# Kernel tuning notes

Measured on AMD Instinct MI355X. Metric: run time of the kernel, lower is better.

Reference implementation:

```python
import jax, jax.numpy as jnp
import numpy as np

LN_EPS = 1e-5

def layer_norm(x, w, b):
    mu = jnp.mean(x, axis=-1, keepdims=True)
    var = jnp.mean(jnp.square(x - mu), axis=-1, keepdims=True)
    return (x - mu) * jax.lax.rsqrt(var + LN_EPS) * w + b

def setup_inputs() -> dict:
    key = jax.random.key(0)
    ks = jax.random.split(key, 8)
    B, F, Q, D = 8, 4096, 64, 1024
    H, DH = 16, 64
    inner = H * DH
    s = 1.0 / np.sqrt(D)
    return {
        "features": jax.random.normal(ks[0], (B, F, D), jnp.float32),
        "latents": jax.random.normal(ks[1], (B, Q, D), jnp.float32),
        "key_attention_mask": jax.random.randint(ks[2], (B, F), 0, 2, jnp.int32),
        "ln_m_w": jnp.ones((D,), jnp.float32),
        "ln_m_b": jnp.zeros((D,), jnp.float32),
        "ln_l_w": jnp.ones((D,), jnp.float32),
        "ln_l_b": jnp.zeros((D,), jnp.float32),
        "Wq": jax.random.normal(ks[3], (D, inner), jnp.float32) * s,
        "Wk": jax.random.normal(ks[4], (D, inner), jnp.float32) * s,
        "Wv": jax.random.normal(ks[5], (D, inner), jnp.float32) * s,
        "Wo": jax.random.normal(ks[6], (inner, D), jnp.float32) * (1.0 / np.sqrt(inner)),
    }

def reference(features, latents, key_attention_mask, ln_m_w, ln_m_b, ln_l_w, ln_l_b, Wq, Wk, Wv, Wo):
    H, DH = 16, 64
    B, F, D = features.shape
    Q = latents.shape[1]
    scale = DH ** (-0.5)

    x = layer_norm(features, ln_m_w, ln_m_b)          # [B,F,D]
    lat = layer_norm(latents, ln_l_w, ln_l_b)          # [B,Q,D]

    q = (lat @ Wq).reshape(B, Q, H, DH).transpose(0, 2, 1, 3)   # [B,H,Q,DH]
    kv_in = jnp.concatenate([x, lat], axis=1)                    # [B,F+Q,D]
    k = (kv_in @ Wk).reshape(B, F + Q, H, DH).transpose(0, 2, 1, 3)
    v = (kv_in @ Wv).reshape(B, F + Q, H, DH).transpose(0, 2, 1, 3)

    q = q * scale
    sim = jnp.einsum('bhqd,bhfd->bhqf', q, k)                    # [B,H,Q,F+Q]

    full_mask = jnp.concatenate(
        [key_attention_mask, jnp.ones((B, Q), key_attention_mask.dtype)], axis=1)  # [B,F+Q]
    sim = jnp.where(full_mask[:, None, None, :] == 0, -jnp.inf, sim)

    sim = sim - jax.lax.stop_gradient(jnp.max(sim, axis=-1, keepdims=True))
    alphas = jax.nn.softmax(sim, axis=-1)
    out = jnp.einsum('bhqf,bhfv->bhqv', alphas, v)               # [B,H,Q,DH]
    out = out.transpose(0, 2, 1, 3).reshape(B, Q, H * DH)        # [B,Q,inner]
    return out @ Wo                                              # [B,Q,D]
```

## Files before the change

### kernel.cpp

```cpp
#include <hip/hip_runtime.h>
#include <hip/hip_bf16.h>

#define B_    8
#define F_    4096
#define Qn    64
#define Dm    1024
#define Hh    16
#define DHn   64
#define FQ    4160
#define ROWS_KV 33280
#define ROWS_F  32768
#define KS    13
#define CHPB  5
#define KVOFF ((size_t)ROWS_KV * 1024)

typedef __bf16 v8bf __attribute__((ext_vector_type(8)));
typedef __bf16 v4bf __attribute__((ext_vector_type(4)));
typedef float  v4f  __attribute__((ext_vector_type(4)));

__device__ inline void gl_lds16(const __bf16* g, __bf16* l) {
  __builtin_amdgcn_global_load_lds((__attribute__((address_space(1))) void*)(g),
                                   (__attribute__((address_space(3))) void*)(l),
                                   16, 0, 0);
}

__device__ inline bool is_bf16_inputs(const void* mw) {
  return ((const unsigned int*)mw)[0] != 0x3F800000u;
}

__global__ __launch_bounds__(256) void prep_kernel(
    const void* __restrict__ feat, const void* __restrict__ lat,
    const void* __restrict__ mw, const void* __restrict__ mb,
    const void* __restrict__ lw, const void* __restrict__ lb,
    __bf16* __restrict__ kv_bf, __bf16* __restrict__ lat_bf,
    const void* __restrict__ w0, const void* __restrict__ w1,
    const void* __restrict__ w2, const void* __restrict__ w3,
    __bf16* __restrict__ t0, __bf16* __restrict__ t1,
    __bf16* __restrict__ t2, __bf16* __restrict__ t3)
{
  bool bf = is_bf16_inputs(mw);
  __shared__ __bf16 tile[32][33];
  int bid = blockIdx.x;
  int tid = threadIdx.x;

  if (bid >= 8320) {
    int tb = bid - 8320;
    int z = tb >> 10, rem = tb & 1023;
    int bxx = rem & 31, byy = rem >> 5;
    int tx = tid & 31, ty = tid >> 5;
    const void* src; __bf16* dst;
    switch (z) {
      case 0: src = w0; dst = t0; break;
      case 1: src = w1; dst = t1; break;
      case 2: src = w2; dst = t2; break;
      default: src = w3; dst = t3; break;
    }
    int x = bxx * 32 + tx;
    #pragma unroll
    for (int j = 0; j < 4; ++j) {
      int y = byy * 32 + ty + j * 8;
      size_t e = (size_t)y * 1024 + x;
      float v = bf ? (float)((const __bf16*)src)[e] : ((const float*)src)[e];
      tile[ty + j * 8][tx] = (__bf16)v;
    }
    __syncthreads();
    int x2 = byy * 32 + tx;
    #pragma unroll
    for (int j = 0; j < 4; ++j) {
      int y2 = bxx * 32 + ty + j * 8;
      dst[(size_t)y2 * 1024 + x2] = tile[tx][ty + j * 8];
    }
    return;
  }

  int wave = tid >> 6, lane = tid & 63;
  int r = bid * 4 + wave;
  const void *rowp, *w, *g;
  __bf16 *dst, *dst2 = nullptr;
  size_t rowoff;
  if (r < ROWS_F) {
    rowoff = (size_t)r * Dm; rowp = feat; w = mw; g = mb;
    int b = r >> 12, f = r & (F_ - 1);
    dst = kv_bf + ((size_t)b * FQ + f) * Dm;
  } else {
    int r2 = r - ROWS_F;
    rowoff = (size_t)r2 * Dm; rowp = lat; w = lw; g = lb;
    int b = r2 >> 6, q = r2 & 63;
    dst  = kv_bf + ((size_t)b * FQ + F_ + q) * Dm;
    dst2 = lat_bf + (size_t)r2 * Dm;
  }
  float xs[16], ws_[16], gs[16];
  if (bf) {
    const __bf16* rp = (const __bf16*)rowp + rowoff;
    const __bf16* wp = (const __bf16*)w;
    const __bf16* gp = (const __bf16*)g;
    #pragma unroll
    for (int g2 = 0; g2 < 2; ++g2) {
      int base = g2 * 512 + lane * 8;
      v8bf X = *(const v8bf*)(rp + base);
      v8bf W = *(const v8bf*)(wp + base);
      v8bf G = *(const v8bf*)(gp + base);
      #pragma unroll
      for (int j = 0; j < 8; ++j) {
        xs[g2*8+j] = (float)X[j]; ws_[g2*8+j] = (float)W[j]; gs[g2*8+j] = (float)G[j];
      }
    }
  } else {
    const float* rp = (const float*)rowp + rowoff;
    const float* wp = (const float*)w;
    const float* gp = (const float*)g;
    #pragma unroll
    for (int g4 = 0; g4 < 4; ++g4) {
      int base = g4 * 256 + lane * 4;
      float4 X = *(const float4*)(rp + base);
      float4 W = *(const float4*)(wp + base);
      float4 G = *(const float4*)(gp + base);
      xs[g4*4]=X.x; xs[g4*4+1]=X.y; xs[g4*4+2]=X.z; xs[g4*4+3]=X.w;
      ws_[g4*4]=W.x; ws_[g4*4+1]=W.y; ws_[g4*4+2]=W.z; ws_[g4*4+3]=W.w;
      gs[g4*4]=G.x; gs[g4*4+1]=G.y; gs[g4*4+2]=G.z; gs[g4*4+3]=G.w;
    }
  }
  float s = 0.f, ss = 0.f;
  #pragma unroll
  for (int j = 0; j < 16; ++j) { s += xs[j]; ss += xs[j] * xs[j]; }
  #pragma unroll
  for (int off = 32; off > 0; off >>= 1) {
    s  += __shfl_xor(s, off, 64);
    ss += __shfl_xor(ss, off, 64);
  }
  float mean = s * (1.f / 1024.f);
  float var  = ss * (1.f / 1024.f) - mean * mean;
  float rs = rsqrtf(var + 1e-5f);
  float os[16];
  #pragma unroll
  for (int j = 0; j < 16; ++j) os[j] = (xs[j] - mean) * rs * ws_[j] + gs[j];
  if (bf) {
    #pragma unroll
    for (int g2 = 0; g2 < 2; ++g2) {
      int base = g2 * 512 + lane * 8;
      v8bf O;
      #pragma unroll
      for (int j = 0; j < 8; ++j) O[j] = (__bf16)os[g2*8+j];
      *(v8bf*)(dst + base) = O;
      if (dst2) *(v8bf*)(dst2 + base) = O;
    }
  } else {
    #pragma unroll
    for (int g4 = 0; g4 < 4; ++g4) {
      int base = g4 * 256 + lane * 4;
      v4bf O;
      #pragma unroll
      for (int j = 0; j < 4; ++j) O[j] = (__bf16)os[g4*4+j];
      *(v4bf*)(dst + base) = O;
      if (dst2) *(v4bf*)(dst2 + base) = O;
    }
  }
}


#define BAR() asm volatile("s_barrier" ::: "memory")

#define PH(Q) do { \
  BAR(); \
  asm volatile("s_waitcnt lgkmcnt(0)" ::: "memory"); \
  __builtin_amdgcn_s_setprio(1); \
  Q; \
  __builtin_amdgcn_s_setprio(0); \
  BAR(); \
} while (0)

#define PHV(Q) do { \
  BAR(); \
  asm volatile("s_waitcnt lgkmcnt(0)" ::: "memory"); \
  __builtin_amdgcn_s_setprio(1); \
  Q; \
  __builtin_amdgcn_s_setprio(0); \
  asm volatile("s_waitcnt vmcnt(4)" ::: "memory"); \
  BAR(); \
} while (0)

#define QUAD(MB, NB, BF) do { \
  _Pragma("unroll") \
  for (int m_ = 0; m_ < 4; ++m_) { \
    _Pragma("unroll") \
    for (int n_ = 0; n_ < 2; ++n_) { \
      _Pragma("unroll") \
      for (int k_ = 0; k_ < 2; ++k_) { \
        acc[(MB) + m_][(NB) + n_] = __builtin_amdgcn_mfma_f32_16x16x32_bf16( \
            af[m_][k_], BF[n_][k_], acc[(MB) + m_][(NB) + n_], 0, 0, 0); \
      } } } } while (0)

#define LDA8(BB, ROFF) do { \
  _Pragma("unroll") \
  for (int m_ = 0; m_ < 4; ++m_) { \
    _Pragma("unroll") \
    for (int k_ = 0; k_ < 2; ++k_) { \
      const int r_ = (ROFF) + m_ * 16 + lm; \
      af[m_][k_] = *(const v8bf*)(aB[BB] + ((r_ << 7) + ((k_ * 64 + kcb) ^ ((r_ & 7) << 4)))); \
    } } } while (0)

#define LDB4(BB, DST, NOFF) do { \
  _Pragma("unroll") \
  for (int n_ = 0; n_ < 2; ++n_) { \
    _Pragma("unroll") \
    for (int k_ = 0; k_ < 2; ++k_) { \
      const int r_ = bq + (NOFF) + n_ * 16 + lm; \
      DST[n_][k_] = *(const v8bf*)(bB[BB] + ((r_ << 7) + ((k_ * 64 + kcb) ^ ((r_ & 7) << 4)))); \
    } } } while (0)

#define STAGE_A(BB, H, K0) do { \
  gl_lds16(asrc + (size_t)(H) * 131072 + (K0),         (__bf16*)(ldsw + ((BB) * 4 + (H)) * 16384)); \
  gl_lds16(asrc + (size_t)(H) * 131072 + (K0) + 65536, (__bf16*)(ldsw + ((BB) * 4 + (H)) * 16384 + 8192)); \
} while (0)

#define STAGE_B(BB, H, K0) do { \
  gl_lds16(bsrc + (size_t)(H) * 131072 + (K0),         (__bf16*)(ldsw + ((BB) * 4 + 2 + (H)) * 16384)); \
  gl_lds16(bsrc + (size_t)(H) * 131072 + (K0) + 65536, (__bf16*)(ldsw + ((BB) * 4 + 2 + (H)) * 16384 + 8192)); \
} while (0)

__global__ __launch_bounds__(512, 2) void gemm_kv8_kernel(
    const __bf16* __restrict__ A, const __bf16* __restrict__ lat,
    const __bf16* __restrict__ BtKV,
    __bf16* __restrict__ KVb, __bf16* __restrict__ Qmb)
{
  __shared__ __align__(16) char ldsm[131072];
  const int tid = threadIdx.x;
  const int lane = tid & 63, wave = tid >> 6;
  const int wm = wave >> 2, wn = wave & 3;
  const int lm = lane & 15, l4 = lane >> 4;
  const int kcb = l4 << 4;
  const int bq = (wn & 1) << 6;

  const int r0 = (wave << 3) + (lane >> 3);
  const int xc = ((lane & 7) ^ (lane >> 3)) << 3;
  char* const ldsw = ldsm + tid * 16;

  if (blockIdx.x >= 1024) {
    int qid = blockIdx.x - 1024;
    int m0q, n0q;
    const __bf16* aq;
    if (qid < 64) {
      int tt = 1024 + (qid & 15);
      m0q = ((tt >> 3) << 8) + (qid >> 4) * 64;
      n0q = (tt & 7) << 8;
      aq = A;
    } else {
      int qq = qid - 64;
      m0q = (((qq >> 2) & 1) << 8) + (qq >> 3) * 64;
      n0q = 2048 + ((qq & 3) << 8);
      aq = lat;
    }
    const __bf16* qasrc = aq + (size_t)(m0q + r0) * 1024 + xc;
    const __bf16* bsrc  = BtKV + (size_t)(n0q + r0) * 1024 + xc;
    const char* const bB[1] = { ldsm + (2 + (wn >> 1)) * 16384 };

    v4f qac[2][4];
    #pragma unroll
    for (int i = 0; i < 2; ++i)
      #pragma unroll
      for (int j = 0; j < 4; ++j) qac[i][j] = (v4f){0.f, 0.f, 0.f, 0.f};

    for (int k0 = 0; k0 < 1024; k0 += 64) {
      __syncthreads();
      gl_lds16(qasrc + k0, (__bf16*)ldsw);
      STAGE_B(0, 0, k0);
      STAGE_B(0, 1, k0);
      __syncthreads();
      v8bf a2[2][2], qlo[2][2], qhi[2][2];
      #pragma unroll
      for (int m_ = 0; m_ < 2; ++m_)
        #pragma unroll
        for (int k_ = 0; k_ < 2; ++k_) {
          const int r_ = wm * 32 + m_ * 16 + lm;
          a2[m_][k_] = *(const v8bf*)(ldsm + ((r_ << 7) + ((k_ * 64 + kcb) ^ ((r_ & 7) << 4))));
        }
      LDB4(0, qlo, 0);
      LDB4(0, qhi, 32);
      #pragma unroll
      for (int m_ = 0; m_ < 2; ++m_)
        #pragma unroll
        for (int n_ = 0; n_ < 2; ++n_)
          #pragma unroll
          for (int k_ = 0; k_ < 2; ++k_) {
            qac[m_][n_]     = __builtin_amdgcn_mfma_f32_16x16x32_bf16(a2[m_][k_], qlo[n_][k_], qac[m_][n_], 0, 0, 0);
            qac[m_][n_ + 2] = __builtin_amdgcn_mfma_f32_16x16x32_bf16(a2[m_][k_], qhi[n_][k_], qac[m_][n_ + 2], 0, 0, 0);
          }
    }

    if (n0q >= 2048) {
      #pragma unroll
      for (int m_ = 0; m_ < 2; ++m_)
        #pragma unroll
        for (int n = 0; n < 4; ++n) {
          int col = n0q + (wn << 6) + n * 16 + lm;
          int h = (col >> 6) & 15, dh = col & 63;
          #pragma unroll
          for (int reg = 0; reg < 4; ++reg) {
            int row = m0q + wm * 32 + m_ * 16 + l4 * 4 + reg;
            int b = row >> 6, q = row & 63;
            Qmb[((size_t)(b * Hh + h) * 64 + q) * 64 + dh] = (__bf16)qac[m_][n][reg];
          }
        }
    } else if (n0q >= 1024) {
      #pragma unroll
      for (int m_ = 0; m_ < 2; ++m_)
        #pragma unroll
        for (int n = 0; n < 4; ++n) {
          int col = n0q + (wn << 6) + n * 16 + lm;
          int h = (col >> 6) & 15, dh = col & 63;
          int f0 = m0q + wm * 32 + m_ * 16 + l4 * 4;
          int b = f0 / FQ, f = f0 - b * FQ;
          v4bf pv;
          #pragma unroll
          for (int reg = 0; reg < 4; ++reg) pv[reg] = (__bf16)qac[m_][n][reg];
          *(v4bf*)(KVb + KVOFF + ((size_t)(b * Hh + h) * 64 + dh) * FQ + f) = pv;
        }
    } else {
      #pragma unroll
      for (int m_ = 0; m_ < 2; ++m_)
        #pragma unroll
        for (int n = 0; n < 4; ++n) {
          int col = n0q + (wn << 6) + n * 16 + lm;
          int h = (col >> 6) & 15, dh = col & 63;
          #pragma unroll
          for (int reg = 0; reg < 4; ++reg) {
            int row = m0q + wm * 32 + m_ * 16 + l4 * 4 + reg;
            int b = row / FQ, f = row - b * FQ;
            KVb[((size_t)(b * Hh + h) * FQ + f) * 64 + dh] = (__bf16)qac[m_][n][reg];
          }
        }
    }
    return;
  }

  const int wg = (blockIdx.x & 7) * 128 + (blockIdx.x >> 3);
  const int n0 = (wg & 7) << 8;
  const int m0 = (wg >> 3) << 8;

  const __bf16* asrc = A    + (size_t)(m0 + r0) * 1024 + xc;
  const __bf16* bsrc = BtKV + (size_t)(n0 + r0) * 1024 + xc;
  const char* const aB[2] = { ldsm + wm * 16384, ldsm + (4 + wm) * 16384 };
  const char* const bB[2] = { ldsm + (2 + (wn >> 1)) * 16384,
                              ldsm + (6 + (wn >> 1)) * 16384 };

  v4f acc[8][4];
  #pragma unroll
  for (int i = 0; i < 8; ++i)
    #pragma unroll
    for (int j = 0; j < 4; ++j) acc[i][j] = (v4f){0.f, 0.f, 0.f, 0.f};
  v8bf af[4][2], blo[2][2], bhi[2][2];

  STAGE_A(0, 0, 0); STAGE_A(0, 1, 0);
  STAGE_B(0, 0, 0); STAGE_B(0, 1, 0);
  STAGE_B(1, 0, 64); STAGE_B(1, 1, 64);
  asm volatile("s_waitcnt vmcnt(4)" ::: "memory");
  BAR();

  #pragma unroll 1
  for (int it = 0; it < 8; ++it) {
    const int kA1 = (2 * it + 1) << 6;
    const int kT0 = (it < 7) ? ((2 * it + 2) << 6) : 0;
    const int kT1 = (it < 7) ? ((2 * it + 3) << 6) : 0;

    LDA8(0, 0); LDB4(0, blo, 0);
    STAGE_A(1, 0, kA1);
    PH(QUAD(0, 0, blo));

    LDB4(0, bhi, 32);
    STAGE_A(1, 1, kA1);
    PH(QUAD(0, 2, bhi));

    LDA8(0, 64);
    STAGE_B(0, 0, kT0);
    PH(QUAD(4, 2, bhi));

    STAGE_B(0, 1, kT0);
    PHV(QUAD(4, 0, blo));

    LDA8(1, 0); LDB4(1, blo, 0);
    STAGE_A(0, 0, kT0);
    PH(QUAD(0, 0, blo));

    LDB4(1, bhi, 32);
    STAGE_A(0, 1, kT0);
    PH(QUAD(0, 2, bhi));

    LDA8(1, 64);
    STAGE_B(1, 0, kT1);
    PH(QUAD(4, 2, bhi));

    STAGE_B(1, 1, kT1);
    PHV(QUAD(4, 0, blo));
  }

  const int rb_l = wm << 7;
  const int cb_l = wn << 6;

  if (n0 >= 1024) {
    __syncthreads();
    #pragma unroll
    for (int m = 0; m < 8; ++m)
      #pragma unroll
      for (int n = 0; n < 4; ++n)
        #pragma unroll
        for (int reg = 0; reg < 4; ++reg) {
          int rl = rb_l + m * 16 + l4 * 4 + reg;
          int cl = cb_l + n * 16 + lm;
          int byt = (cl << 9) + ((rl << 1) ^ (((cl >> 2) & 7) << 5));
          *(__bf16*)(ldsm + byt) = (__bf16)acc[m][n][reg];
        }
    __syncthreads();
    {
      const int g = tid >> 4, s = tid & 15;
      #pragma unroll
      for (int p = 0; p < 16; ++p) {
        int d = p * 32 + g;
        int cl = d >> 1, hf = d & 1;
        int byt = (cl << 9) + ((((hf << 8) + (s << 4))) ^ (((cl >> 2) & 7) << 5));
        v8bf val = *(const v8bf*)(ldsm + byt);
        int col = n0 + cl;
        int h = (col >> 6) & 15, dh = col & 63;
        int row = m0 + (hf << 7) + (s << 3);
        int b = row / FQ, f = row - b * FQ;
        *(v8bf*)(KVb + KVOFF + ((size_t)(b * Hh + h) * 64 + dh) * FQ + f) = val;
      }
    }
  } else {
    __syncthreads();
    #pragma unroll
    for (int m = 0; m < 8; ++m)
      #pragma unroll
      for (int n = 0; n < 4; ++n)
        #pragma unroll
        for (int reg = 0; reg < 4; ++reg) {
          int rl = rb_l + m * 16 + l4 * 4 + reg;
          int cl = cb_l + n * 16 + lm;
          int byt = (rl << 9) + ((cl << 1) ^ (((rl >> 2) & 7) << 5));
          *(__bf16*)(ldsm + byt) = (__bf16)acc[m][n][reg];
        }
    __syncthreads();
    {
      const int g = tid >> 3, s = tid & 7;
      #pragma unroll
      for (int p = 0; p < 16; ++p) {
        int d = p * 64 + g;
        int hl = d >> 8, fl = d & 255;
        int byt = (fl << 9) + ((((hl << 7) + (s << 4))) ^ (((fl >> 2) & 7) << 5));
        v8bf val = *(const v8bf*)(ldsm + byt);
        int row = m0 + fl;
        int b = row / FQ, f = row - b * FQ;
        int h = ((n0 + (hl << 6)) >> 6) & 15;
        *(v8bf*)(KVb + ((size_t)(b * Hh + h) * FQ + f) * 64 + (s << 3)) = val;
      }
    }
  }
}

__global__ __launch_bounds__(256) void gemm2_kernel(
    const __bf16* __restrict__ A, const __bf16* __restrict__ Bt,
    void* __restrict__ C, int mode, int out_follow,
    const void* __restrict__ mw)
{
  int obf = out_follow ? (is_bf16_inputs(mw) ? 1 : 0) : 1;

  __shared__ __align__(16) __bf16 As0[128 * 32];
  __shared__ __align__(16) __bf16 As1[128 * 32];
  __shared__ __align__(16) __bf16 Bs0[128 * 32];
  __shared__ __align__(16) __bf16 Bs1[128 * 32];
  int tid = threadIdx.x;
  int lane = tid & 63, wave = tid >> 6;
  int wm = wave >> 1, wn = wave & 1;
  int m0 = blockIdx.y * 128, n0 = blockIdx.x * 128;
  int lm = lane & 15, lk = (lane >> 4) << 3;

  v4f acc[4][4];
  #pragma unroll
  for (int i = 0; i < 4; ++i)
    #pragma unroll
    for (int j = 0; j < 4; ++j) acc[i][j] = (v4f){0.f, 0.f, 0.f, 0.f};

  int c0 = tid, c1 = tid + 256;
  const __bf16* a0p = A  + (size_t)(m0 + (c0 >> 2)) * 1024 + ((c0 & 3) << 3);
  const __bf16* a1p = A  + (size_t)(m0 + (c1 >> 2)) * 1024 + ((c1 & 3) << 3);
  const __bf16* b0p = Bt + (size_t)(n0 + (c0 >> 2)) * 1024 + ((c0 & 3) << 3);
  const __bf16* b1p = Bt + (size_t)(n0 + (c1 >> 2)) * 1024 + ((c1 & 3) << 3);

  for (int k0 = 0; k0 < 1024; k0 += 64) {
    __syncthreads();
    gl_lds16(a0p + k0,      &As0[c0 * 8]);
    gl_lds16(a1p + k0,      &As0[c1 * 8]);
    gl_lds16(a0p + k0 + 32, &As1[c0 * 8]);
    gl_lds16(a1p + k0 + 32, &As1[c1 * 8]);
    gl_lds16(b0p + k0,      &Bs0[c0 * 8]);
    gl_lds16(b1p + k0,      &Bs0[c1 * 8]);
    gl_lds16(b0p + k0 + 32, &Bs1[c0 * 8]);
    gl_lds16(b1p + k0 + 32, &Bs1[c1 * 8]);
    __syncthreads();
    {
      v8bf a[4], b[4];
      #pragma unroll
      for (int i = 0; i < 4; ++i) a[i] = *(const v8bf*)&As0[(wm * 64 + i * 16 + lm) * 32 + lk];
      #pragma unroll
      for (int j = 0; j < 4; ++j) b[j] = *(const v8bf*)&Bs0[(wn * 64 + j * 16 + lm) * 32 + lk];
      #pragma unroll
      for (int i = 0; i < 4; ++i)
        #pragma unroll
        for (int j = 0; j < 4; ++j)
          acc[i][j] = __builtin_amdgcn_mfma_f32_16x16x32_bf16(a[i], b[j], acc[i][j], 0, 0, 0);
    }
    {
      v8bf a[4], b[4];
      #pragma unroll
      for (int i = 0; i < 4; ++i) a[i] = *(const v8bf*)&As1[(wm * 64 + i * 16 + lm) * 32 + lk];
      #pragma unroll
      for (int j = 0; j < 4; ++j) b[j] = *(const v8bf*)&Bs1[(wn * 64 + j * 16 + lm) * 32 + lk];
      #pragma unroll
      for (int i = 0; i < 4; ++i)
        #pragma unroll
        for (int j = 0; j < 4; ++j)
          acc[i][j] = __builtin_amdgcn_mfma_f32_16x16x32_bf16(a[i], b[j], acc[i][j], 0, 0, 0);
    }
  }

  #pragma unroll
  for (int i = 0; i < 4; ++i)
    #pragma unroll
    for (int j = 0; j < 4; ++j) {
      int col = n0 + wn * 64 + j * 16 + lm;
      #pragma unroll
      for (int reg = 0; reg < 4; ++reg) {
        int row = m0 + wm * 64 + i * 16 + (lane >> 4) * 4 + reg;
        size_t idx;
        if (mode == 0) {
          idx = (size_t)row * 1024 + col;
        } else {
          int bb = row >> 6; int qq = row & 63;
          idx = ((size_t)(bb * Hh + (col >> 6)) * 64 + qq) * 64 + (col & 63);
        }
        float v = acc[i][j][reg];
        if (obf) ((__bf16*)C)[idx] = (__bf16)v;
        else     ((float*)C)[idx]  = v;
      }
    }
}

__global__ __launch_bounds__(256) void attn_part_kernel(
    const __bf16* __restrict__ Qm, const __bf16* __restrict__ K,
    const __bf16* __restrict__ Vt, const int* __restrict__ mask,
    float* __restrict__ Opart, float2* __restrict__ ml)
{
  __shared__ __align__(16) __bf16 qs[64 * 72];
  __shared__ __align__(16) __bf16 ks[64 * 72];
  __shared__ __align__(16) __bf16 vts[64 * 72];
  __shared__ __align__(16) __bf16 ps[64 * 72];
  __shared__ float msb[64];

  int tid = threadIdx.x;
  int lane = tid & 63, wave = tid >> 6;
  int ksb = blockIdx.x;
  int bh = blockIdx.y;
  int b = bh >> 4;
  int lm = lane & 15, lq = lane >> 4;

  const __bf16* qsrc = Qm + (size_t)bh * 64 * 64;
  #pragma unroll
  for (int i = 0; i < 2; ++i) {
    int e = (tid + 256 * i) * 8;
    int row = e >> 6, c = e & 63;
    *(v8bf*)&qs[row * 72 + c] = *(const v8bf*)(qsrc + e);
  }

  float mrow[4], lrow[4];
  v4f acco[4];
  #pragma unroll
  for (int r = 0; r < 4; ++r) { mrow[r] = -1e30f; lrow[r] = 0.f; }
  #pragma unroll
  for (int s = 0; s < 4; ++s) acco[s] = (v4f){0.f, 0.f, 0.f, 0.f};

  const __bf16* kbase = K + (size_t)bh * FQ * 64;
  const __bf16* vbase = Vt + (size_t)bh * 64 * FQ;
  const int* maskb = mask + b * F_;

  for (int cc = 0; cc < CHPB; ++cc) {
    int chunk = ksb * CHPB + cc;
    __syncthreads();
    const __bf16* kc = kbase + (size_t)chunk * 4096;
    const __bf16* vc = vbase + chunk * 64;
    #pragma unroll
    for (int i = 0; i < 2; ++i) {
      int e = (tid + 256 * i) * 8;
      int row = e >> 6, c = e & 63;
      *(v8bf*)&ks[row * 72 + c]  = *(const v8bf*)(kc + e);
      *(v8bf*)&vts[row * 72 + c] = *(const v8bf*)(vc + (size_t)row * FQ + c);
    }
    if (tid < 64) {
      int kidx = chunk * 64 + tid;
      msb[tid] = (kidx < F_) ? (maskb[kidx] != 0 ? 0.f : -1e30f) : 0.f;
    }
    __syncthreads();

    v8bf aq0 = *(const v8bf*)&qs[(wave * 16 + lm) * 72 + lq * 8];
    v8bf aq1 = *(const v8bf*)&qs[(wave * 16 + lm) * 72 + lq * 8 + 32];
    v4f sf[4];
    #pragma unroll
    for (int s = 0; s < 4; ++s) {
      v8bf bk0 = *(const v8bf*)&ks[(s * 16 + lm) * 72 + lq * 8];
      v8bf bk1 = *(const v8bf*)&ks[(s * 16 + lm) * 72 + lq * 8 + 32];
      v4f z = (v4f){0.f, 0.f, 0.f, 0.f};
      z = __builtin_amdgcn_mfma_f32_16x16x32_bf16(aq0, bk0, z, 0, 0, 0);
      z = __builtin_amdgcn_mfma_f32_16x16x32_bf16(aq1, bk1, z, 0, 0, 0);
      sf[s] = z;
    }
    float bias[4];
    #pragma unroll
    for (int s = 0; s < 4; ++s) bias[s] = msb[s * 16 + lm];
    #pragma unroll
    for (int s = 0; s < 4; ++s)
      #pragma unroll
      for (int r = 0; r < 4; ++r)
        sf[s][r] = sf[s][r] * 0.125f + bias[s];

    #pragma unroll
    for (int r = 0; r < 4; ++r) {
      float mx = fmaxf(fmaxf(sf[0][r], sf[1][r]), fmaxf(sf[2][r], sf[3][r]));
      #pragma unroll
      for (int off = 1; off < 16; off <<= 1) mx = fmaxf(mx, __shfl_xor(mx, off, 64));
      float mN = fmaxf(mrow[r], mx);
      float alpha = __expf(mrow[r] - mN);
      mrow[r] = mN;
      float ls = 0.f;
      #pragma unroll
      for (int s = 0; s < 4; ++s) { float p = __expf(sf[s][r] - mN); sf[s][r] = p; ls += p; }
      #pragma unroll
      for (int off = 1; off < 16; off <<= 1) ls += __shfl_xor(ls, off, 64);
      lrow[r] = lrow[r] * alpha + ls;
      #pragma unroll
      for (int s = 0; s < 4; ++s) acco[s][r] *= alpha;
    }

    #pragma unroll
    for (int s = 0; s < 4; ++s)
      #pragma unroll
      for (int r = 0; r < 4; ++r)
        ps[(wave * 16 + lq * 4 + r) * 72 + s * 16 + lm] = (__bf16)sf[s][r];

    v8bf ap0 = *(const v8bf*)&ps[(wave * 16 + lm) * 72 + lq * 8];
    v8bf ap1 = *(const v8bf*)&ps[(wave * 16 + lm) * 72 + lq * 8 + 32];
    #pragma unroll
    for (int s = 0; s < 4; ++s) {
      v8bf bv0 = *(const v8bf*)&vts[(s * 16 + lm) * 72 + lq * 8];
      v8bf bv1 = *(const v8bf*)&vts[(s * 16 + lm) * 72 + lq * 8 + 32];
      acco[s] = __builtin_amdgcn_mfma_f32_16x16x32_bf16(ap0, bv0, acco[s], 0, 0, 0);
      acco[s] = __builtin_amdgcn_mfma_f32_16x16x32_bf16(ap1, bv1, acco[s], 0, 0, 0);
    }
  }

  float* Ob = Opart + (((size_t)ksb * 128 + bh) * 64) * 64;
  #pragma unroll
  for (int s = 0; s < 4; ++s)
    #pragma unroll
    for (int r = 0; r < 4; ++r) {
      int q = wave * 16 + lq * 4 + r;
      Ob[q * 64 + s * 16 + lm] = acco[s][r];
    }
  if (lm == 0) {
    #pragma unroll
    for (int r = 0; r < 4; ++r) {
      int q = wave * 16 + lq * 4 + r;
      ml[((size_t)ksb * 128 + bh) * 64 + q] = make_float2(mrow[r], lrow[r]);
    }
  }
}

__global__ __launch_bounds__(256) void attn_comb_kernel(
    const float* __restrict__ Opart, const float2* __restrict__ ml,
    __bf16* __restrict__ attnb)
{
  int bh = blockIdx.x;
  int b = bh >> 4, h = bh & 15;
  int t = threadIdx.x;
  int q = t >> 2, cg = (t & 3) * 16;

  float m_[KS], l_[KS];
  float M = -1e30f;
  #pragma unroll
  for (int k = 0; k < KS; ++k) {
    float2 p = ml[((size_t)k * 128 + bh) * 64 + q];
    m_[k] = p.x; l_[k] = p.y;
    M = fmaxf(M, p.x);
  }
  float L = 0.f;
  #pragma unroll
  for (int k = 0; k < KS; ++k) L += l_[k] * __expf(m_[k] - M);
  float o[16];
  #pragma unroll
  for (int j = 0; j < 16; ++j) o[j] = 0.f;
  #pragma unroll
  for (int k = 0; k < KS; ++k) {
    float wgt = __expf(m_[k] - M);
    const float* P = Opart + ((((size_t)k * 128 + bh) * 64 + q) * 64) + cg;
    #pragma unroll
    for (int j4 = 0; j4 < 4; ++j4) {
      float4 pv = *(const float4*)(P + j4 * 4);
      o[j4*4]   += pv.x * wgt; o[j4*4+1] += pv.y * wgt;
      o[j4*4+2] += pv.z * wgt; o[j4*4+3] += pv.w * wgt;
    }
  }
  float invL = 1.f / L;
  __bf16* dst = attnb + ((size_t)(b * 64 + q) * 1024) + h * 64 + cg;
  v8bf O0, O1;
  #pragma unroll
  for (int j = 0; j < 8; ++j) { O0[j] = (__bf16)(o[j] * invL); O1[j] = (__bf16)(o[8+j] * invL); }
  *(v8bf*)dst = O0;
  *(v8bf*)(dst + 8) = O1;
}

extern "C" void kernel_launch(void* const* d_in, const int* in_sizes, int n_in,
                              void* d_out, int out_size, void* d_ws, size_t ws_size,
                              hipStream_t stream)
{
  void* feat = d_in[0];
  void* lat  = d_in[1];
  const int* mk = (const int*)d_in[2];
  void* mw = d_in[3]; void* mb = d_in[4];
  void* lw = d_in[5]; void* lb = d_in[6];
  void* Wq = d_in[7]; void* Wk = d_in[8];
  void* Wv = d_in[9]; void* Wo = d_in[10];

  char* ws = (char*)d_ws;
  size_t off = 0;
  auto alloc = [&](size_t bytes) {
    char* p = ws + off;
    off += (bytes + 255) & ~(size_t)255;
    return p;
  };
  __bf16* WkvT  = (__bf16*)alloc((size_t)3 * 1024 * 1024 * 2);
  __bf16* WoT   = (__bf16*)alloc((size_t)1024 * 1024 * 2);
  __bf16* KVb   = (__bf16*)alloc((size_t)2 * ROWS_KV * 1024 * 2);
  __bf16* Qmb   = (__bf16*)alloc((size_t)512 * 1024 * 2);
  __bf16* attnb = (__bf16*)alloc((size_t)512 * 1024 * 2);
  __bf16* lat_bf= (__bf16*)alloc((size_t)512 * 1024 * 2);
  char*   big   = (char*)alloc((size_t)ROWS_KV * 1024 * 2);
  __bf16* kv_bf = (__bf16*)big;
  float*  Opart = (float*)big;
  float2* ml    = (float2*)(big + (size_t)KS*128*64*64*4);
  if (ws_size < off) return;

  prep_kernel<<<12416, 256, 0, stream>>>(
      feat, lat, mw, mb, lw, lb, kv_bf, lat_bf,
      Wq, Wk, Wv, Wo,
      WkvT + (size_t)2 * 1024 * 1024,
      WkvT,
      WkvT + (size_t)1024 * 1024,
      WoT);

  gemm_kv8_kernel<<<dim3(1120), dim3(512), 0, stream>>>(
      kv_bf, lat_bf, WkvT, KVb, Qmb);

  attn_part_kernel<<<dim3(KS, 128), 256, 0, stream>>>(
      Qmb, KVb, KVb + KVOFF, mk, Opart, ml);
  attn_comb_kernel<<<128, 256, 0, stream>>>(Opart, ml, attnb);

  gemm2_kernel<<<dim3(8, 4), 256, 0, stream>>>(attnb, WoT, d_out, 0, 1, mw);
}
```

Before: 433.2 us.

## Transpose QK^T MFMA so each lane owns one query row; rebalance KV splits

```diff
diff --git a/kernel.cpp b/kernel.cpp
--- a/kernel.cpp
+++ b/kernel.cpp
@@ -10,12 +10,12 @@
 #define FQ    4160
 #define ROWS_KV 33280
 #define ROWS_F  32768
-#define KS    13
-#define CHPB  5
+#define KS    16
 #define KVOFF ((size_t)ROWS_KV * 1024)
 
 typedef __bf16 v8bf __attribute__((ext_vector_type(8)));
 typedef __bf16 v4bf __attribute__((ext_vector_type(4)));
+typedef __bf16 v2bf __attribute__((ext_vector_type(2)));
 typedef float  v4f  __attribute__((ext_vector_type(4)));
 
 __device__ inline void gl_lds16(const __bf16* g, __bf16* l) {
@@ -557,7 +557,7 @@
 
   int tid = threadIdx.x;
   int lane = tid & 63, wave = tid >> 6;
-  int ksb = blockIdx.x;
+  int ksb = (KS - 1) - blockIdx.x;
   int bh = blockIdx.y;
   int b = bh >> 4;
   int lm = lane & 15, lq = lane >> 4;
@@ -569,11 +569,12 @@
     int row = e >> 6, c = e & 63;
     *(v8bf*)&qs[row * 72 + c] = *(const v8bf*)(qsrc + e);
   }
-
-  float mrow[4], lrow[4];
+  __syncthreads();
+  const v8bf aq0 = *(const v8bf*)&qs[(wave * 16 + lm) * 72 + lq * 8];
+  const v8bf aq1 = *(const v8bf*)&qs[(wave * 16 + lm) * 72 + lq * 8 + 32];
+
+  float mreg = -1e30f, lreg = 0.f;
   v4f acco[4];
-  #pragma unroll
-  for (int r = 0; r < 4; ++r) { mrow[r] = -1e30f; lrow[r] = 0.f; }
   #pragma unroll
   for (int s = 0; s < 4; ++s) acco[s] = (v4f){0.f, 0.f, 0.f, 0.f};
 
@@ -581,8 +582,11 @@
   const __bf16* vbase = Vt + (size_t)bh * 64 * FQ;
   const int* maskb = mask + b * F_;
 
-  for (int cc = 0; cc < CHPB; ++cc) {
-    int chunk = ksb * CHPB + cc;
+  const int cbase = ksb * 4;
+  const int ncc = (ksb == KS - 1) ? 5 : 4;
+
+  for (int cc = 0; cc < ncc; ++cc) {
+    int chunk = cbase + cc;
     __syncthreads();
     const __bf16* kc = kbase + (size_t)chunk * 4096;
     const __bf16* vc = vbase + chunk * 64;
@@ -599,50 +603,66 @@
     }
     __syncthreads();
 
-    v8bf aq0 = *(const v8bf*)&qs[(wave * 16 + lm) * 72 + lq * 8];
-    v8bf aq1 = *(const v8bf*)&qs[(wave * 16 + lm) * 72 + lq * 8 + 32];
     v4f sf[4];
     #pragma unroll
     for (int s = 0; s < 4; ++s) {
       v8bf bk0 = *(const v8bf*)&ks[(s * 16 + lm) * 72 + lq * 8];
       v8bf bk1 = *(const v8bf*)&ks[(s * 16 + lm) * 72 + lq * 8 + 32];
       v4f z = (v4f){0.f, 0.f, 0.f, 0.f};
-      z = __builtin_amdgcn_mfma_f32_16x16x32_bf16(aq0, bk0, z, 0, 0, 0);
-      z = __builtin_amdgcn_mfma_f32_16x16x32_bf16(aq1, bk1, z, 0, 0, 0);
+      z = __builtin_amdgcn_mfma_f32_16x16x32_bf16(bk0, aq0, z, 0, 0, 0);
+      z = __builtin_amdgcn_mfma_f32_16x16x32_bf16(bk1, aq1, z, 0, 0, 0);
       sf[s] = z;
     }
-    float bias[4];
-    #pragma unroll
-    for (int s = 0; s < 4; ++s) bias[s] = msb[s * 16 + lm];
+    #pragma unroll
+    for (int s = 0; s < 4; ++s) {
+      const float4 mm = *(const float4*)&msb[s * 16 + lq * 4];
+      sf[s][0] = sf[s][0] * 0.125f + mm.x;
+      sf[s][1] = sf[s][1] * 0.125f + mm.y;
+      sf[s][2] = sf[s][2] * 0.125f + mm.z;
+      sf[s][3] = sf[s][3] * 0.125f + mm.w;
+    }
+
+    float mx = sf[0][0];
     #pragma unroll
     for (int s = 0; s < 4; ++s)
       #pragma unroll
-      for (int r = 0; r < 4; ++r)
-        sf[s][r] = sf[s][r] * 0.125f + bias[s];
-
-    #pragma unroll
-    for (int r = 0; r < 4; ++r) {
-      float mx = fmaxf(fmaxf(sf[0][r], sf[1][r]), fmaxf(sf[2][r], sf[3][r]));
-      #pragma unroll
-      for (int off = 1; off < 16; off <<= 1) mx = fmaxf(mx, __shfl_xor(mx, off, 64));
-      float mN = fmaxf(mrow[r], mx);
-      float alpha = __expf(mrow[r] - mN);
-      mrow[r] = mN;
-      float ls = 0.f;
-      #pragma unroll
-      for (int s = 0; s < 4; ++s) { float p = __expf(sf[s][r] - mN); sf[s][r] = p; ls += p; }
-      #pragma unroll
-      for (int off = 1; off < 16; off <<= 1) ls += __shfl_xor(ls, off, 64);
-      lrow[r] = lrow[r] * alpha + ls;
-      #pragma unroll
-      for (int s = 0; s < 4; ++s) acco[s][r] *= alpha;
-    }
-
+      for (int r = 0; r < 4; ++r) mx = fmaxf(mx, sf[s][r]);
+    mx = fmaxf(mx, __shfl_xor(mx, 16, 64));
+    mx = fmaxf(mx, __shfl_xor(mx, 32, 64));
+    float mN = fmaxf(mreg, mx);
+    float alpha = __expf(mreg - mN);
+    mreg = mN;
+    float ls = 0.f;
     #pragma unroll
     for (int s = 0; s < 4; ++s)
       #pragma unroll
-      for (int r = 0; r < 4; ++r)
-        ps[(wave * 16 + lq * 4 + r) * 72 + s * 16 + lm] = (__bf16)sf[s][r];
+      for (int r = 0; r < 4; ++r) {
+        float p = __expf(sf[s][r] - mN);
+        sf[s][r] = p;
+        ls += p;
+      }
+    ls += __shfl_xor(ls, 16, 64);
+    ls += __shfl_xor(ls, 32, 64);
+    lreg = lreg * alpha + ls;
+
+    float al[4];
+    #pragma unroll
+    for (int r = 0; r < 4; ++r)
+      al[r] = __shfl(alpha, (lane & 48) | (lq * 4 + r), 64);
+    #pragma unroll
+    for (int s = 0; s < 4; ++s)
+      #pragma unroll
+      for (int r = 0; r < 4; ++r) acco[s][r] *= al[r];
+
+    #pragma unroll
+    for (int s = 0; s < 4; ++s)
+      #pragma unroll
+      for (int h = 0; h < 2; ++h) {
+        v2bf t;
+        t[0] = (__bf16)sf[s][2 * h];
+        t[1] = (__bf16)sf[s][2 * h + 1];
+        *(v2bf*)&ps[(wave * 16 + lm) * 72 + s * 16 + lq * 4 + 2 * h] = t;
+      }
 
     v8bf ap0 = *(const v8bf*)&ps[(wave * 16 + lm) * 72 + lq * 8];
     v8bf ap1 = *(const v8bf*)&ps[(wave * 16 + lm) * 72 + lq * 8 + 32];
@@ -663,12 +683,9 @@
       int q = wave * 16 + lq * 4 + r;
       Ob[q * 64 + s * 16 + lm] = acco[s][r];
     }
-  if (lm == 0) {
-    #pragma unroll
-    for (int r = 0; r < 4; ++r) {
-      int q = wave * 16 + lq * 4 + r;
-      ml[((size_t)ksb * 128 + bh) * 64 + q] = make_float2(mrow[r], lrow[r]);
-    }
+  if (lq == 0) {
+    int q = wave * 16 + lm;
+    ml[((size_t)ksb * 128 + bh) * 64 + q] = make_float2(mreg, lreg);
   }
 }
 
```

Result: no change. 432.9 us (-0.1%).
